# Optimization experiments

Hardware: AMD Instinct MI355X
Metric: run time of the kernel (lower is better)

## Reference

```python
import jax, jax.numpy as jnp
import numpy as np

HIDDEN = 640
NQ = 10      # query heads
NKV = 2      # kv heads
HD = HIDDEN // NQ   # 64
GROUPS = NQ // NKV  # 5
THETA = 500000.0
EPS = 1e-6


def rmsnorm(x, g):
    rms = jnp.sqrt(jnp.mean(x * x, axis=-1, keepdims=True) + EPS)
    return x / rms * g


def bitlinear(x, w, g):
    """RMSNorm + ternary weight / int8 activation fake-quant + GEMM + rescale."""
    x = rmsnorm(x, g)
    alpha = jnp.maximum(jnp.mean(jnp.abs(w)), 1e-10)
    w_q = jnp.clip(jnp.round(w / alpha), -1.0, 1.0)
    w_q = w + jax.lax.stop_gradient(w_q - w)            # STE
    gamma = jnp.maximum(jnp.max(jnp.abs(x), axis=-1, keepdims=True), 1e-10)
    x_q = jnp.clip(jnp.round(x * 127.0 / gamma), -128.0, 127.0)
    x_q = x + jax.lax.stop_gradient(x_q - x)            # STE
    return (x_q @ w_q.T) * (alpha * gamma / 127.0)


def rope_tables(L):
    # half-dim cos/sin tables [L, HD//2]; equivalent to the torch code's
    # repeat_interleave followed by [..., ::2] slicing.
    freqs = 1.0 / THETA ** (jnp.arange(0, HD, 2, dtype=jnp.float32) / HD)
    ang = jnp.arange(L, dtype=jnp.float32)[:, None] * freqs[None, :]
    return jnp.cos(ang), jnp.sin(ang)


def apply_rope(x, cos, sin):
    # x: [B,H,L,D]; cos/sin: [L,D/2] broadcast over B,H
    x1 = x[..., ::2]
    x2 = x[..., 1::2]
    o1 = x1 * cos - x2 * sin
    o2 = x2 * cos + x1 * sin
    return jnp.stack([o1, o2], axis=-1).reshape(x.shape)


def setup_inputs() -> dict:
    key = jax.random.key(0)
    ks = jax.random.split(key, 6)
    B, L = 32, 512
    x = jax.random.normal(ks[0], (B, L, HIDDEN), dtype=jnp.float32)
    s_h = 1.0 / np.sqrt(HIDDEN)
    q_w = jax.random.normal(ks[1], (NQ * HD, HIDDEN), dtype=jnp.float32) * s_h
    k_w = jax.random.normal(ks[2], (NKV * HD, HIDDEN), dtype=jnp.float32) * s_h
    v_w = jax.random.normal(ks[3], (NKV * HD, HIDDEN), dtype=jnp.float32) * s_h
    o_w = jax.random.normal(ks[4], (HIDDEN, NQ * HD), dtype=jnp.float32) * (1.0 / np.sqrt(NQ * HD))
    ones = jnp.ones((HIDDEN,), dtype=jnp.float32)
    return {
        "x": x,
        "norm_w": ones,
        "q_w": q_w, "q_g": ones,
        "k_w": k_w, "k_g": ones,
        "v_w": v_w, "v_g": ones,
        "o_w": o_w, "o_g": jnp.ones((NQ * HD,), dtype=jnp.float32),
    }


def reference(x, norm_w, q_w, q_g, k_w, k_g, v_w, v_g, o_w, o_g):
    B, L, _ = x.shape
    residual = x
    h = rmsnorm(x, norm_w)
    q = bitlinear(h, q_w, q_g).reshape(B, L, NQ, HD).transpose(0, 2, 1, 3)
    k = bitlinear(h, k_w, k_g).reshape(B, L, NKV, HD).transpose(0, 2, 1, 3)
    v = bitlinear(h, v_w, v_g).reshape(B, L, NKV, HD).transpose(0, 2, 1, 3)
    cos, sin = rope_tables(L)
    q = apply_rope(q, cos, sin)
    k = apply_rope(k, cos, sin)
    k = jnp.repeat(k, GROUPS, axis=1)   # [B,NQ,L,HD]
    v = jnp.repeat(v, GROUPS, axis=1)
    scale = 1.0 / np.sqrt(HD).astype(np.float32)
    attn = jnp.einsum("bhqd,bhkd->bhqk", q, k) * scale
    attn = jax.nn.softmax(attn, axis=-1)
    out = jnp.einsum("bhqk,bhkd->bhqd", attn, v)
    out = out.transpose(0, 2, 1, 3).reshape(B, L, NQ * HD)
    return bitlinear(out, o_w, o_g) + residual
```

## Files before the change

kernel.cpp:

```cpp
#include <hip/hip_runtime.h>
#include <math.h>
#include <stdint.h>

#define HIDDEN 640
#define NTOK   16384
#define LSEQ   512
#define BATCH  32
#define NQH    10
#define NKVH   2
#define HDIM   64
#define GROUPS 5

typedef int      int4v  __attribute__((ext_vector_type(4)));
typedef int      int16v __attribute__((ext_vector_type(16)));
typedef _Float16 f16x8  __attribute__((ext_vector_type(8)));
typedef _Float16 f16x2  __attribute__((ext_vector_type(2)));
typedef float    f32x4  __attribute__((ext_vector_type(4)));

__device__ __forceinline__ float wred_sum(float v){
  #pragma unroll
  for (int m=1;m<64;m<<=1) v += __shfl_xor(v,m);
  return v;
}
__device__ __forceinline__ float wred_max(float v){
  #pragma unroll
  for (int m=1;m<64;m<<=1) v = fmaxf(v,__shfl_xor(v,m));
  return v;
}

__device__ __forceinline__ int frag_flat(int m, int k){
  return (((m>>5)*20 + (k>>5))<<10) + (((((k>>4)&1)<<5) | (m&31))<<4) + (k&15);
}

__global__ __launch_bounds__(256) void absum4_kernel(
    const float* __restrict__ w0, const float* __restrict__ w1,
    const float* __restrict__ w2, const float* __restrict__ w3,
    float* __restrict__ sums){
  const float* w; int n;
  switch(blockIdx.y){
    case 0:  w=w0; n=640*640; break;
    case 1:  w=w1; n=128*640; break;
    case 2:  w=w2; n=128*640; break;
    default: w=w3; n=640*640; break;
  }
  __shared__ float red[256];
  int tid = threadIdx.x;
  float s = 0.f;
  for (int i = blockIdx.x*256 + tid; i < n; i += gridDim.x*256) s += fabsf(w[i]);
  red[tid] = s; __syncthreads();
  for (int off=128; off>0; off>>=1){ if (tid<off) red[tid]+=red[tid+off]; __syncthreads(); }
  if (tid==0) atomicAdd(&sums[blockIdx.y], red[0]);
}

__global__ __launch_bounds__(256) void wquant4_kernel(
    const float* __restrict__ w0, const float* __restrict__ w1,
    const float* __restrict__ w2, const float* __restrict__ w3,
    int8_t* __restrict__ o0, int8_t* __restrict__ o1,
    int8_t* __restrict__ o2, int8_t* __restrict__ o3,
    const float* __restrict__ sums){
  const float* w; int8_t* o; int n;
  switch(blockIdx.y){
    case 0:  w=w0; o=o0; n=640*640; break;
    case 1:  w=w1; o=o1; n=128*640; break;
    case 2:  w=w2; o=o2; n=128*640; break;
    default: w=w3; o=o3; n=640*640; break;
  }
  float alpha = fmaxf(sums[blockIdx.y]/(float)n, 1e-10f);
  float inva  = 1.0f/alpha;
  int i = blockIdx.x*256 + threadIdx.x;
  if (i < n){
    float t = rintf(w[i]*inva);
    t = fminf(1.f, fmaxf(-1.f, t));
    int nr = i/640;
    int kc = i - nr*640;
    o[frag_flat(nr, kc)] = (int8_t)t;
  }
}

__global__ __launch_bounds__(256) void token_prep_kernel(
    const float* __restrict__ x, const float* __restrict__ nw,
    const float* __restrict__ qg, const float* __restrict__ kg, const float* __restrict__ vg,
    int8_t* __restrict__ xqq, int8_t* __restrict__ xqk, int8_t* __restrict__ xqv,
    float* __restrict__ gq, float* __restrict__ gk, float* __restrict__ gv){
  int lane = threadIdx.x & 63;
  int m = blockIdx.x*4 + (threadIdx.x>>6);
  const float* xr = x + (size_t)m*HIDDEN;
  int abase = ((m>>5)*20480) + ((m&31)<<4)
            + ((lane>>5)<<10) + (((lane>>4)&1)<<9) + (lane&15);
  float xv[10], h[10];
  float ss = 0.f;
  #pragma unroll
  for (int j=0;j<10;j++){ float t = xr[lane + 64*j]; xv[j]=t; ss += t*t; }
  float inv1 = 1.0f/sqrtf(wred_sum(ss)*(1.0f/HIDDEN) + 1e-6f);
  float ss2 = 0.f;
  #pragma unroll
  for (int j=0;j<10;j++){ float t = xv[j]*inv1*nw[lane+64*j]; h[j]=t; ss2 += t*t; }
  float inv2 = 1.0f/sqrtf(wred_sum(ss2)*(1.0f/HIDDEN) + 1e-6f);

  const float* gs[3] = {qg, kg, vg};
  int8_t* outs[3] = {xqq, xqk, xqv};
  float* gams[3] = {gq, gk, gv};
  #pragma unroll
  for (int s=0;s<3;s++){
    const float* g = gs[s];
    float t[10], amax = 0.f;
    #pragma unroll
    for (int j=0;j<10;j++){ float v = h[j]*inv2*g[lane+64*j]; t[j]=v; amax = fmaxf(amax, fabsf(v)); }
    float gamma = fmaxf(wred_max(amax), 1e-10f);
    float sc = 127.0f/gamma;
    int8_t* dst = outs[s] + abase;
    #pragma unroll
    for (int j=0;j<10;j++){
      float v = rintf(t[j]*sc);
      v = fminf(127.f, fmaxf(-128.f, v));
      dst[j*2048] = (int8_t)v;
    }
    if (lane==0) gams[s][m] = gamma;
  }
}

__global__ __launch_bounds__(256) void o_prep_kernel(const _Float16* __restrict__ ao,
    const float* __restrict__ og, int8_t* __restrict__ xqo, float* __restrict__ go){
  int lane = threadIdx.x & 63;
  int m = blockIdx.x*4 + (threadIdx.x>>6);
  const _Float16* xr = ao + (size_t)m*HIDDEN;
  int abase = ((m>>5)*20480) + ((m&31)<<4)
            + ((lane>>5)<<10) + (((lane>>4)&1)<<9) + (lane&15);
  float xv[10];
  float ss = 0.f;
  #pragma unroll
  for (int j=0;j<10;j++){ float t = (float)xr[lane + 64*j]; xv[j]=t; ss += t*t; }
  float inv = 1.0f/sqrtf(wred_sum(ss)*(1.0f/HIDDEN) + 1e-6f);
  float t[10], amax = 0.f;
  #pragma unroll
  for (int j=0;j<10;j++){ float v = xv[j]*inv*og[lane+64*j]; t[j]=v; amax = fmaxf(amax, fabsf(v)); }
  float gamma = fmaxf(wred_max(amax), 1e-10f);
  float sc = 127.0f/gamma;
  int8_t* dst = xqo + abase;
  #pragma unroll
  for (int j=0;j<10;j++){
    float v = rintf(t[j]*sc);
    v = fminf(127.f, fmaxf(-128.f, v));
    dst[j*2048] = (int8_t)v;
  }
  if (lane==0) go[m] = gamma;
}

__device__ __forceinline__ void gemm_core(
    const int8_t* __restrict__ xq, const int8_t* __restrict__ wqf,
    int m0, int n0, int lane, int16v& acc0, int16v& acc1){
  const int8_t* a0 = xq  + (size_t)(m0>>5)*20480 + (lane<<4);
  const int8_t* b0 = wqf + (size_t)(n0>>5)*20480 + (lane<<4);
  const int8_t* b1 = b0 + 20480;
  #pragma unroll
  for (int kb=0; kb<20; kb++){
    int4v a  = *(const int4v*)(a0 + (kb<<10));
    int4v v0 = *(const int4v*)(b0 + (kb<<10));
    int4v v1 = *(const int4v*)(b1 + (kb<<10));
    acc0 = __builtin_amdgcn_mfma_i32_32x32x32_i8(a, v0, acc0, 0, 0, 0);
    acc1 = __builtin_amdgcn_mfma_i32_32x32x32_i8(a, v1, acc1, 0, 0, 0);
  }
}

__global__ __launch_bounds__(256) void qkv_gemm_kernel(
    const int8_t* __restrict__ xq_q, const float* __restrict__ g_q, const int8_t* __restrict__ wq_q,
    const int8_t* __restrict__ xq_k, const float* __restrict__ g_k, const int8_t* __restrict__ wq_k,
    const int8_t* __restrict__ xq_v, const float* __restrict__ g_v, const int8_t* __restrict__ wq_v,
    const float* __restrict__ sums,
    _Float16* __restrict__ qbuf, _Float16* __restrict__ kbuf, _Float16* __restrict__ vbuf){
  __shared__ _Float16 Tr[4][64][40];
  int bx = blockIdx.x;
  const int8_t *xq, *wq; const float* gam; _Float16* outh;
  int n0, aidx, nheads, mode; float inv_nw, vscale;
  if (bx < 10){ xq=xq_q; wq=wq_q; gam=g_q; outh=qbuf; n0=bx*64;      aidx=0; inv_nw=1.0f/409600.f; nheads=NQH;  mode=1; vscale=0.18033688011110918f; }
  else if (bx < 12){ xq=xq_k; wq=wq_k; gam=g_k; outh=kbuf; n0=(bx-10)*64; aidx=1; inv_nw=1.0f/81920.f; nheads=NKVH; mode=1; vscale=1.0f; }
  else { xq=xq_v; wq=wq_v; gam=g_v; outh=vbuf; n0=(bx-12)*64; aidx=2; inv_nw=1.0f/81920.f; nheads=NKVH; mode=2; vscale=1.0f; }

  int lane = threadIdx.x & 63;
  int w    = threadIdx.x >> 6;
  int m0   = blockIdx.y*128 + w*32;
  int half = lane >> 5, lan5 = lane & 31;

  int16v acc0 = {0}, acc1 = {0};
  gemm_core(xq, wq, m0, n0, lane, acc0, acc1);

  float alpha = fmaxf(sums[aidx]*inv_nw, 1e-10f);
  float fr0 = 0.f, fr1 = 0.f;
  if (mode == 1){
    int d0 = (lan5) & ~1;
    int d1 = (32 + lan5) & ~1;
    fr0 = __expf(-(float)d0*(1.0f/64.0f)*13.122363377404328f);
    fr1 = __expf(-(float)d1*(1.0f/64.0f)*13.122363377404328f);
  }

  #pragma unroll
  for (int reg=0; reg<16; reg++){
    int ml = (reg&3) + 8*(reg>>2) + 4*half;
    int m = m0 + ml;
    float sc = alpha*gam[m]*(1.0f/127.0f);
    float v0 = (float)acc0[reg]*sc;
    float v1 = (float)acc1[reg]*sc;
    if (mode == 1){
      int b = m >> 9, l = m & 511;
      int head = n0 >> 6;
      float p0 = __shfl_xor(v0, 1);
      float p1 = __shfl_xor(v1, 1);
      float sn0, cs0, sn1, cs1;
      __sincosf((float)l*fr0, &sn0, &cs0);
      __sincosf((float)l*fr1, &sn1, &cs1);
      if (lane & 1){ v0 = v0*cs0 + p0*sn0;  v1 = v1*cs1 + p1*sn1; }
      else         { v0 = v0*cs0 - p0*sn0;  v1 = v1*cs1 - p1*sn1; }
      _Float16* dst = outh + ((((size_t)b*nheads + head)*LSEQ + l)<<6);
      dst[lan5]      = (_Float16)(v0*vscale);
      dst[32 + lan5] = (_Float16)(v1*vscale);
    } else {
      Tr[w][lan5][ml]      = (_Float16)v0;
      Tr[w][32 + lan5][ml] = (_Float16)v1;
    }
  }
  if (mode == 2){
    int b = m0 >> 9, l0 = m0 & 511;
    int head = n0 >> 6;
    f16x8 r0 = *(const f16x8*)&Tr[w][lane][0];
    f16x8 r1 = *(const f16x8*)&Tr[w][lane][8];
    f16x8 r2 = *(const f16x8*)&Tr[w][lane][16];
    f16x8 r3 = *(const f16x8*)&Tr[w][lane][24];
    _Float16* dst = outh + (((size_t)b*nheads + head)*HDIM + lane)*LSEQ + l0;
    ((f16x8*)dst)[0] = r0;
    ((f16x8*)dst)[1] = r1;
    ((f16x8*)dst)[2] = r2;
    ((f16x8*)dst)[3] = r3;
  }
}

__global__ __launch_bounds__(256) void out_gemm_kernel(
    const int8_t* __restrict__ xq, const float* __restrict__ gam,
    const int8_t* __restrict__ wq, const float* __restrict__ sums,
    const float* __restrict__ resid, float* __restrict__ outf){
  int lane = threadIdx.x & 63;
  int w    = threadIdx.x >> 6;
  int m0   = blockIdx.y*128 + w*32;
  int n0   = blockIdx.x*64;
  int half = lane >> 5, lan5 = lane & 31;

  int16v acc0 = {0}, acc1 = {0};
  gemm_core(xq, wq, m0, n0, lane, acc0, acc1);

  float alpha = fmaxf(sums[3]*(1.0f/409600.f), 1e-10f);
  #pragma unroll
  for (int reg=0; reg<16; reg++){
    int m = m0 + (reg&3) + 8*(reg>>2) + 4*half;
    float sc = alpha*gam[m]*(1.0f/127.0f);
    size_t ofs = (size_t)m*HIDDEN;
    outf[ofs + n0 + lan5]      = (float)acc0[reg]*sc + resid[ofs + n0 + lan5];
    outf[ofs + n0 + 32 + lan5] = (float)acc1[reg]*sc + resid[ofs + n0 + 32 + lan5];
  }
}

__device__ __forceinline__ int kv_addr(int row, int chunk){
  return (row<<6) + (((chunk ^ (row&7)))<<3);
}

__device__ __forceinline__ void softmax_half(
    const f32x4* S, float& m, f32x4& lacc, f32x4* O, int quad, bool first,
    f16x8& pf0, f16x8& pf1){
  float t0 = fmaxf(fmaxf(S[0][0],S[0][1]), fmaxf(S[0][2],S[0][3]));
  float t1 = fmaxf(fmaxf(S[1][0],S[1][1]), fmaxf(S[1][2],S[1][3]));
  float t2 = fmaxf(fmaxf(S[2][0],S[2][1]), fmaxf(S[2][2],S[2][3]));
  float t3 = fmaxf(fmaxf(S[3][0],S[3][1]), fmaxf(S[3][2],S[3][3]));
  float tmax = fmaxf(fmaxf(t0,t1), fmaxf(t2,t3));
  tmax = fmaxf(tmax, __shfl_xor(tmax, 16));
  tmax = fmaxf(tmax, __shfl_xor(tmax, 32));
  float p[16];
  if (first || __any(tmax > 8.0f)){
    float delta = first ? tmax : fmaxf(tmax, 0.0f);
    m += delta;
    float af = exp2f(-delta);
    #pragma unroll
    for (int r=0;r<4;r++){
      float afr = __shfl(af, (quad<<2)+r);
      lacc[r] *= afr;
      O[0][r]*=afr; O[1][r]*=afr; O[2][r]*=afr; O[3][r]*=afr;
    }
    #pragma unroll
    for (int nt=0;nt<4;nt++){
      #pragma unroll
      for (int j=0;j<4;j++) p[(nt<<2)+j] = exp2f(S[nt][j] - delta);
    }
  } else {
    #pragma unroll
    for (int nt=0;nt<4;nt++){
      #pragma unroll
      for (int j=0;j<4;j++) p[(nt<<2)+j] = exp2f(S[nt][j]);
    }
  }
  uint32_t W[4][2];
  #pragma unroll
  for (int nt=0;nt<4;nt++){
    W[nt][0] = __builtin_bit_cast(uint32_t,
                 __builtin_amdgcn_cvt_pkrtz(p[(nt<<2)+0], p[(nt<<2)+1]));
    W[nt][1] = __builtin_bit_cast(uint32_t,
                 __builtin_amdgcn_cvt_pkrtz(p[(nt<<2)+2], p[(nt<<2)+3]));
  }
  #pragma unroll
  for (int pp=0;pp<2;pp++){
    asm volatile("v_permlane32_swap_b32 %0, %1" : "+v"(W[0][pp]), "+v"(W[1][pp]));
    asm volatile("v_permlane32_swap_b32 %0, %1" : "+v"(W[2][pp]), "+v"(W[3][pp]));
    asm volatile("v_permlane16_swap_b32 %0, %1" : "+v"(W[0][pp]), "+v"(W[1][pp]));
    asm volatile("v_permlane16_swap_b32 %0, %1" : "+v"(W[2][pp]), "+v"(W[3][pp]));
  }
  union { uint32_t u[4]; f16x8 v; } a, b;
  a.u[0]=W[0][0]; a.u[1]=W[0][1]; a.u[2]=W[1][0]; a.u[3]=W[1][1];
  b.u[0]=W[2][0]; b.u[1]=W[2][1]; b.u[2]=W[3][0]; b.u[3]=W[3][1];
  pf0 = a.v; pf1 = b.v;
}

__global__ __launch_bounds__(256,3) void attn_mfma_kernel(
    const _Float16* __restrict__ q, const _Float16* __restrict__ k,
    const _Float16* __restrict__ vt, _Float16* __restrict__ o){
  __shared__ _Float16 Ks[2][64*64];
  __shared__ _Float16 Vs[2][64*64];
  int tid  = threadIdx.x;
  int wv   = tid >> 6, lane = tid & 63;
  int quad = lane >> 4, c = lane & 15;
  int h = blockIdx.y, b = blockIdx.z;
  int hk = h / GROUPS;
  int qrow0 = blockIdx.x*128 + wv*32;

  const _Float16* qb = q + ((size_t)((b*NQH+h)*LSEQ) + qrow0 + c)*HDIM + quad*8;
  f16x8 qa0 = *(const f16x8*)qb;
  f16x8 qa1 = *(const f16x8*)(qb + 32);
  f16x8 qb0 = *(const f16x8*)(qb + 16*HDIM);
  f16x8 qb1 = *(const f16x8*)(qb + 16*HDIM + 32);

  const _Float16* kbase = k  + (size_t)((b*NKVH+hk)*LSEQ)*HDIM;
  const _Float16* vbase = vt + (size_t)((b*NKVH+hk)*HDIM)*LSEQ;

  int srow = tid >> 3, schunk = tid & 7;
  const _Float16* kg0 = kbase + (size_t)srow*HDIM      + schunk*8;
  const _Float16* kg1 = kbase + (size_t)(srow+32)*HDIM + schunk*8;
  const _Float16* vg0 = vbase + (size_t)srow*LSEQ      + schunk*8;
  const _Float16* vg1 = vbase + (size_t)(srow+32)*LSEQ + schunk*8;
  int ka0 = kv_addr(srow,    schunk);
  int ka1 = kv_addr(srow+32, schunk);

  {
    f16x8 t0 = *(const f16x8*)kg0;
    f16x8 t1 = *(const f16x8*)kg1;
    f16x8 t2 = *(const f16x8*)vg0;
    f16x8 t3 = *(const f16x8*)vg1;
    *(f16x8*)&Ks[0][ka0] = t0;
    *(f16x8*)&Ks[0][ka1] = t1;
    *(f16x8*)&Vs[0][ka0] = t2;
    *(f16x8*)&Vs[0][ka1] = t3;
  }

  f32x4 O0[4] = {{0,0,0,0},{0,0,0,0},{0,0,0,0},{0,0,0,0}};
  f32x4 O1[4] = {{0,0,0,0},{0,0,0,0},{0,0,0,0},{0,0,0,0}};
  f32x4 lacc0 = {0,0,0,0}, lacc1 = {0,0,0,0};
  float m0s = 0.f, m1s = 0.f;
  const f16x8 ones = {(_Float16)1.f,(_Float16)1.f,(_Float16)1.f,(_Float16)1.f,
                      (_Float16)1.f,(_Float16)1.f,(_Float16)1.f,(_Float16)1.f};
  f16x8 pk0, pk1, pv0, pv1;

  for (int kt=0; kt<8; kt++){
    __syncthreads();
    int cur = kt & 1, nxt = cur ^ 1;
    if (kt < 7){
      pk0 = *(const f16x8*)(kg0 + (size_t)(kt+1)*64*HDIM);
      pk1 = *(const f16x8*)(kg1 + (size_t)(kt+1)*64*HDIM);
      pv0 = *(const f16x8*)(vg0 + (kt+1)*64);
      pv1 = *(const f16x8*)(vg1 + (kt+1)*64);
    }
    f32x4 S0[4], S1[4];
    __builtin_amdgcn_s_setprio(1);
    #pragma unroll
    for (int nt=0; nt<4; nt++){
      int row = (nt<<4) + c;
      f16x8 kf0 = *(const f16x8*)&Ks[cur][kv_addr(row, quad)];
      f16x8 kf1 = *(const f16x8*)&Ks[cur][kv_addr(row, quad+4)];
      f32x4 s = {-m0s,-m0s,-m0s,-m0s};
      s = __builtin_amdgcn_mfma_f32_16x16x32_f16(kf0, qa0, s, 0,0,0);
      s = __builtin_amdgcn_mfma_f32_16x16x32_f16(kf1, qa1, s, 0,0,0);
      S0[nt] = s;
      f32x4 s2 = {-m1s,-m1s,-m1s,-m1s};
      s2 = __builtin_amdgcn_mfma_f32_16x16x32_f16(kf0, qb0, s2, 0,0,0);
      s2 = __builtin_amdgcn_mfma_f32_16x16x32_f16(kf1, qb1, s2, 0,0,0);
      S1[nt] = s2;
    }
    __builtin_amdgcn_s_setprio(0);
    f16x8 pf00, pf01, pf10, pf11;
    softmax_half(S0, m0s, lacc0, O0, quad, kt==0, pf00, pf01);
    softmax_half(S1, m1s, lacc1, O1, quad, kt==0, pf10, pf11);
    __builtin_amdgcn_s_setprio(1);
    lacc0 = __builtin_amdgcn_mfma_f32_16x16x32_f16(pf00, ones, lacc0, 0,0,0);
    lacc0 = __builtin_amdgcn_mfma_f32_16x16x32_f16(pf01, ones, lacc0, 0,0,0);
    lacc1 = __builtin_amdgcn_mfma_f32_16x16x32_f16(pf10, ones, lacc1, 0,0,0);
    lacc1 = __builtin_amdgcn_mfma_f32_16x16x32_f16(pf11, ones, lacc1, 0,0,0);
    #pragma unroll
    for (int nt=0;nt<4;nt++){
      int row = (nt<<4) + c;
      f16x8 vf0 = *(const f16x8*)&Vs[cur][kv_addr(row, quad)];
      f16x8 vf1 = *(const f16x8*)&Vs[cur][kv_addr(row, quad+4)];
      O0[nt] = __builtin_amdgcn_mfma_f32_16x16x32_f16(pf00, vf0, O0[nt], 0,0,0);
      O0[nt] = __builtin_amdgcn_mfma_f32_16x16x32_f16(pf01, vf1, O0[nt], 0,0,0);
      O1[nt] = __builtin_amdgcn_mfma_f32_16x16x32_f16(pf10, vf0, O1[nt], 0,0,0);
      O1[nt] = __builtin_amdgcn_mfma_f32_16x16x32_f16(pf11, vf1, O1[nt], 0,0,0);
    }
    __builtin_amdgcn_s_setprio(0);
    if (kt < 7){
      *(f16x8*)&Ks[nxt][ka0] = pk0;
      *(f16x8*)&Ks[nxt][ka1] = pk1;
      *(f16x8*)&Vs[nxt][ka0] = pv0;
      *(f16x8*)&Vs[nxt][ka1] = pv1;
    }
  }
  #pragma unroll
  for (int r=0;r<4;r++){
    float invl0 = 1.0f/lacc0[r];
    float invl1 = 1.0f/lacc1[r];
    int m0 = (b<<9) + qrow0 + (quad<<2) + r;
    _Float16* d0 = o + (size_t)m0*HIDDEN + (h<<6);
    _Float16* d1 = o + (size_t)(m0+16)*HIDDEN + (h<<6);
    #pragma unroll
    for (int nt=0;nt<4;nt++){
      d0[(nt<<4)+c] = (_Float16)(O0[nt][r]*invl0);
      d1[(nt<<4)+c] = (_Float16)(O1[nt][r]*invl1);
    }
  }
}

extern "C" void kernel_launch(void* const* d_in, const int* in_sizes, int n_in,
                              void* d_out, int out_size, void* d_ws, size_t ws_size,
                              hipStream_t stream){
  (void)in_sizes; (void)n_in; (void)out_size; (void)ws_size;
  const float* x  = (const float*)d_in[0];
  const float* nw = (const float*)d_in[1];
  const float* qw = (const float*)d_in[2];
  const float* qg = (const float*)d_in[3];
  const float* kw = (const float*)d_in[4];
  const float* kg = (const float*)d_in[5];
  const float* vw = (const float*)d_in[6];
  const float* vg = (const float*)d_in[7];
  const float* ow = (const float*)d_in[8];
  const float* og = (const float*)d_in[9];
  float* out = (float*)d_out;

  char* base = (char*)d_ws;
  size_t off = 0;
  auto alloc = [&](size_t nbytes)->void*{
    off = (off + 255) & ~(size_t)255;
    void* p = base + off;
    off += nbytes;
    return p;
  };
  float*  sums = (float*) alloc(4*sizeof(float));
  int8_t* wq_q = (int8_t*)alloc(640*640);
  int8_t* wq_k = (int8_t*)alloc(128*640);
  int8_t* wq_v = (int8_t*)alloc(128*640);
  int8_t* wq_o = (int8_t*)alloc(640*640);
  int8_t* xq_q = (int8_t*)alloc((size_t)NTOK*HIDDEN);
  int8_t* xq_k = (int8_t*)alloc((size_t)NTOK*HIDDEN);
  int8_t* xq_v = (int8_t*)alloc((size_t)NTOK*HIDDEN);
  int8_t* xq_o = (int8_t*)alloc((size_t)NTOK*HIDDEN);
  float*  g_q  = (float*) alloc((size_t)NTOK*4);
  float*  g_k  = (float*) alloc((size_t)NTOK*4);
  float*  g_v  = (float*) alloc((size_t)NTOK*4);
  float*  g_o  = (float*) alloc((size_t)NTOK*4);
  _Float16* qbuf = (_Float16*)alloc((size_t)BATCH*NQH *LSEQ*HDIM*2);
  _Float16* kbuf = (_Float16*)alloc((size_t)BATCH*NKVH*LSEQ*HDIM*2);
  _Float16* vbuf = (_Float16*)alloc((size_t)BATCH*NKVH*LSEQ*HDIM*2);
  _Float16* abuf = (_Float16*)alloc((size_t)NTOK*HIDDEN*2);

  (void)hipMemsetAsync(sums, 0, 4*sizeof(float), stream);
  absum4_kernel<<<dim3(64,4),256,0,stream>>>(qw, kw, vw, ow, sums);
  wquant4_kernel<<<dim3(1600,4),256,0,stream>>>(qw, kw, vw, ow, wq_q, wq_k, wq_v, wq_o, sums);

  token_prep_kernel<<<NTOK/4,256,0,stream>>>(x, nw, qg, kg, vg, xq_q, xq_k, xq_v, g_q, g_k, g_v);

  qkv_gemm_kernel<<<dim3(14,128),256,0,stream>>>(xq_q, g_q, wq_q,
                                                 xq_k, g_k, wq_k,
                                                 xq_v, g_v, wq_v,
                                                 sums, qbuf, kbuf, vbuf);

  attn_mfma_kernel<<<dim3(4,NQH,BATCH),256,0,stream>>>(qbuf, kbuf, vbuf, abuf);

  o_prep_kernel<<<NTOK/4,256,0,stream>>>(abuf, og, xq_o, g_o);
  out_gemm_kernel<<<dim3(10,128),256,0,stream>>>(xq_o, g_o, wq_o, sums, x, out);
}
```

Before: 238.2 us.

## Software-pipeline attention QK and softmax-PV, stage K/V via direct global-to-LDS loads

Restructures the attention loop so the QK^T MFMAs for tile kt overlap the softmax and PV MFMAs of tile kt-1, using a triple-buffered V tile and a deferred max-shift correction term. K/V staging now uses global_load_lds to write straight into shared memory, with a swizzled source address, instead of going through registers. The intent is to hide softmax VALU latency behind MFMA work and to cut register pressure and VGPR round trips on loads. In exchange it uses more LDS and adds extra softmax branching, which may lower occupancy.

After: 266.4 us. 11.8% more time.

```diff
diff --git a/kernel.cpp b/kernel.cpp
--- a/kernel.cpp
+++ b/kernel.cpp
@@ -261,20 +261,30 @@
   return (row<<6) + (((chunk ^ (row&7)))<<3);
 }
 
+__device__ __forceinline__ void gload_lds16(const void* g, void* l){
+  __builtin_amdgcn_global_load_lds(
+      (const __attribute__((address_space(1))) unsigned int*)g,
+      (__attribute__((address_space(3))) unsigned int*)l, 16, 0, 0);
+}
+
 __device__ __forceinline__ void softmax_half(
-    const f32x4* S, float& m, f32x4& lacc, f32x4* O, int quad, bool first,
+    const f32x4* S, float& m, float& dc, f32x4& lacc, f32x4* O, int quad, bool first,
     f16x8& pf0, f16x8& pf1){
-  float t0 = fmaxf(fmaxf(S[0][0],S[0][1]), fmaxf(S[0][2],S[0][3]));
-  float t1 = fmaxf(fmaxf(S[1][0],S[1][1]), fmaxf(S[1][2],S[1][3]));
-  float t2 = fmaxf(fmaxf(S[2][0],S[2][1]), fmaxf(S[2][2],S[2][3]));
-  float t3 = fmaxf(fmaxf(S[3][0],S[3][1]), fmaxf(S[3][2],S[3][3]));
-  float tmax = fmaxf(fmaxf(t0,t1), fmaxf(t2,t3));
+  float t0 = fmaxf(fmaxf(fmaxf(S[0][0],S[0][1]),S[0][2]),S[0][3]);
+  float t1 = fmaxf(fmaxf(fmaxf(S[1][0],S[1][1]),S[1][2]),S[1][3]);
+  float t2 = fmaxf(fmaxf(fmaxf(S[2][0],S[2][1]),S[2][2]),S[2][3]);
+  float t3 = fmaxf(fmaxf(fmaxf(S[3][0],S[3][1]),S[3][2]),S[3][3]);
+  float tmax = fmaxf(fmaxf(fmaxf(t0,t1),t2),t3);
   tmax = fmaxf(tmax, __shfl_xor(tmax, 16));
   tmax = fmaxf(tmax, __shfl_xor(tmax, 32));
+  float D = dc;
+  float teff = tmax - D;
   float p[16];
-  if (first || __any(tmax > 8.0f)){
-    float delta = first ? tmax : fmaxf(tmax, 0.0f);
+  if (first || __any(teff > 8.0f)){
+    float delta = first ? teff : fmaxf(teff, 0.0f);
+    float shift = D + delta;
     m += delta;
+    dc = delta;
     float af = exp2f(-delta);
     #pragma unroll
     for (int r=0;r<4;r++){
@@ -285,9 +295,17 @@
     #pragma unroll
     for (int nt=0;nt<4;nt++){
       #pragma unroll
-      for (int j=0;j<4;j++) p[(nt<<2)+j] = exp2f(S[nt][j] - delta);
+      for (int j=0;j<4;j++) p[(nt<<2)+j] = exp2f(S[nt][j] - shift);
+    }
+  } else if (__any(D != 0.0f)){
+    dc = 0.0f;
+    #pragma unroll
+    for (int nt=0;nt<4;nt++){
+      #pragma unroll
+      for (int j=0;j<4;j++) p[(nt<<2)+j] = exp2f(S[nt][j] - D);
     }
   } else {
+    dc = 0.0f;
     #pragma unroll
     for (int nt=0;nt<4;nt++){
       #pragma unroll
@@ -319,7 +337,7 @@
     const _Float16* __restrict__ q, const _Float16* __restrict__ k,
     const _Float16* __restrict__ vt, _Float16* __restrict__ o){
   __shared__ _Float16 Ks[2][64*64];
-  __shared__ _Float16 Vs[2][64*64];
+  __shared__ _Float16 Vs[3][64*64];
   int tid  = threadIdx.x;
   int wv   = tid >> 6, lane = tid & 63;
   int quad = lane >> 4, c = lane & 15;
@@ -333,46 +351,39 @@
   f16x8 qb0 = *(const f16x8*)(qb + 16*HDIM);
   f16x8 qb1 = *(const f16x8*)(qb + 16*HDIM + 32);
 
-  const _Float16* kbase = k  + (size_t)((b*NKVH+hk)*LSEQ)*HDIM;
-  const _Float16* vbase = vt + (size_t)((b*NKVH+hk)*HDIM)*LSEQ;
-
-  int srow = tid >> 3, schunk = tid & 7;
-  const _Float16* kg0 = kbase + (size_t)srow*HDIM      + schunk*8;
-  const _Float16* kg1 = kbase + (size_t)(srow+32)*HDIM + schunk*8;
-  const _Float16* vg0 = vbase + (size_t)srow*LSEQ      + schunk*8;
-  const _Float16* vg1 = vbase + (size_t)(srow+32)*LSEQ + schunk*8;
-  int ka0 = kv_addr(srow,    schunk);
-  int ka1 = kv_addr(srow+32, schunk);
-
-  {
-    f16x8 t0 = *(const f16x8*)kg0;
-    f16x8 t1 = *(const f16x8*)kg1;
-    f16x8 t2 = *(const f16x8*)vg0;
-    f16x8 t3 = *(const f16x8*)vg1;
-    *(f16x8*)&Ks[0][ka0] = t0;
-    *(f16x8*)&Ks[0][ka1] = t1;
-    *(f16x8*)&Vs[0][ka0] = t2;
-    *(f16x8*)&Vs[0][ka1] = t3;
-  }
+  const char* kbase = (const char*)(k  + (size_t)((b*NKVH+hk)*LSEQ)*HDIM);
+  const char* vbase = (const char*)(vt + (size_t)((b*NKVH+hk)*HDIM)*LSEQ);
+
+  int r7 = lane >> 3, s7 = lane & 7;
+  int cg = s7 ^ r7;
+  size_t koffA = (size_t)(wv*8 + r7)*128  + (size_t)cg*16;
+  size_t koffB = koffA + 32*128;
+  size_t voffA = (size_t)(wv*8 + r7)*1024 + (size_t)cg*16;
+  size_t voffB = voffA + 32*1024;
+
+  #define STAGE_KV(ksl, vsl, t) do{                                          \
+    gload_lds16(kbase + (size_t)(t)*8192 + koffA, &Ks[ksl][wv*512]);         \
+    gload_lds16(kbase + (size_t)(t)*8192 + koffB, &Ks[ksl][2048 + wv*512]);  \
+    gload_lds16(vbase + (size_t)(t)*128  + voffA, &Vs[vsl][wv*512]);         \
+    gload_lds16(vbase + (size_t)(t)*128  + voffB, &Vs[vsl][2048 + wv*512]);  \
+  }while(0)
+
+  STAGE_KV(0, 0, 0);
 
   f32x4 O0[4] = {{0,0,0,0},{0,0,0,0},{0,0,0,0},{0,0,0,0}};
   f32x4 O1[4] = {{0,0,0,0},{0,0,0,0},{0,0,0,0},{0,0,0,0}};
   f32x4 lacc0 = {0,0,0,0}, lacc1 = {0,0,0,0};
-  float m0s = 0.f, m1s = 0.f;
+  float m0s = 0.f, m1s = 0.f, dc0 = 0.f, dc1 = 0.f;
   const f16x8 ones = {(_Float16)1.f,(_Float16)1.f,(_Float16)1.f,(_Float16)1.f,
                       (_Float16)1.f,(_Float16)1.f,(_Float16)1.f,(_Float16)1.f};
-  f16x8 pk0, pk1, pv0, pv1;
-
+  f32x4 Sp0[4], Sp1[4];
+
+  #pragma unroll
   for (int kt=0; kt<8; kt++){
     __syncthreads();
-    int cur = kt & 1, nxt = cur ^ 1;
-    if (kt < 7){
-      pk0 = *(const f16x8*)(kg0 + (size_t)(kt+1)*64*HDIM);
-      pk1 = *(const f16x8*)(kg1 + (size_t)(kt+1)*64*HDIM);
-      pv0 = *(const f16x8*)(vg0 + (kt+1)*64);
-      pv1 = *(const f16x8*)(vg1 + (kt+1)*64);
-    }
-    f32x4 S0[4], S1[4];
+    if (kt < 7) STAGE_KV((kt+1)&1, (kt+1)%3, kt+1);
+    int cur = kt & 1;
+    f32x4 Sn0[4], Sn1[4];
     __builtin_amdgcn_s_setprio(1);
     #pragma unroll
     for (int nt=0; nt<4; nt++){
@@ -382,17 +393,42 @@
       f32x4 s = {-m0s,-m0s,-m0s,-m0s};
       s = __builtin_amdgcn_mfma_f32_16x16x32_f16(kf0, qa0, s, 0,0,0);
       s = __builtin_amdgcn_mfma_f32_16x16x32_f16(kf1, qa1, s, 0,0,0);
-      S0[nt] = s;
+      Sn0[nt] = s;
       f32x4 s2 = {-m1s,-m1s,-m1s,-m1s};
       s2 = __builtin_amdgcn_mfma_f32_16x16x32_f16(kf0, qb0, s2, 0,0,0);
       s2 = __builtin_amdgcn_mfma_f32_16x16x32_f16(kf1, qb1, s2, 0,0,0);
-      S1[nt] = s2;
+      Sn1[nt] = s2;
     }
     __builtin_amdgcn_s_setprio(0);
+    if (kt > 0){
+      int prv = (kt-1)%3;
+      f16x8 pf00, pf01, pf10, pf11;
+      softmax_half(Sp0, m0s, dc0, lacc0, O0, quad, kt==1, pf00, pf01);
+      softmax_half(Sp1, m1s, dc1, lacc1, O1, quad, kt==1, pf10, pf11);
+      __builtin_amdgcn_s_setprio(1);
+      lacc0 = __builtin_amdgcn_mfma_f32_16x16x32_f16(pf00, ones, lacc0, 0,0,0);
+      lacc0 = __builtin_amdgcn_mfma_f32_16x16x32_f16(pf01, ones, lacc0, 0,0,0);
+      lacc1 = __builtin_amdgcn_mfma_f32_16x16x32_f16(pf10, ones, lacc1, 0,0,0);
+      lacc1 = __builtin_amdgcn_mfma_f32_16x16x32_f16(pf11, ones, lacc1, 0,0,0);
+      #pragma unroll
+      for (int nt=0;nt<4;nt++){
+        int row = (nt<<4) + c;
+        f16x8 vf0 = *(const f16x8*)&Vs[prv][kv_addr(row, quad)];
+        f16x8 vf1 = *(const f16x8*)&Vs[prv][kv_addr(row, quad+4)];
+        O0[nt] = __builtin_amdgcn_mfma_f32_16x16x32_f16(pf00, vf0, O0[nt], 0,0,0);
+        O0[nt] = __builtin_amdgcn_mfma_f32_16x16x32_f16(pf01, vf1, O0[nt], 0,0,0);
+        O1[nt] = __builtin_amdgcn_mfma_f32_16x16x32_f16(pf10, vf0, O1[nt], 0,0,0);
+        O1[nt] = __builtin_amdgcn_mfma_f32_16x16x32_f16(pf11, vf1, O1[nt], 0,0,0);
+      }
+      __builtin_amdgcn_s_setprio(0);
+    }
+    #pragma unroll
+    for (int nt=0;nt<4;nt++){ Sp0[nt] = Sn0[nt]; Sp1[nt] = Sn1[nt]; }
+  }
+  {
     f16x8 pf00, pf01, pf10, pf11;
-    softmax_half(S0, m0s, lacc0, O0, quad, kt==0, pf00, pf01);
-    softmax_half(S1, m1s, lacc1, O1, quad, kt==0, pf10, pf11);
-    __builtin_amdgcn_s_setprio(1);
+    softmax_half(Sp0, m0s, dc0, lacc0, O0, quad, false, pf00, pf01);
+    softmax_half(Sp1, m1s, dc1, lacc1, O1, quad, false, pf10, pf11);
     lacc0 = __builtin_amdgcn_mfma_f32_16x16x32_f16(pf00, ones, lacc0, 0,0,0);
     lacc0 = __builtin_amdgcn_mfma_f32_16x16x32_f16(pf01, ones, lacc0, 0,0,0);
     lacc1 = __builtin_amdgcn_mfma_f32_16x16x32_f16(pf10, ones, lacc1, 0,0,0);
@@ -400,21 +436,15 @@
     #pragma unroll
     for (int nt=0;nt<4;nt++){
       int row = (nt<<4) + c;
-      f16x8 vf0 = *(const f16x8*)&Vs[cur][kv_addr(row, quad)];
-      f16x8 vf1 = *(const f16x8*)&Vs[cur][kv_addr(row, quad+4)];
+      f16x8 vf0 = *(const f16x8*)&Vs[1][kv_addr(row, quad)];
+      f16x8 vf1 = *(const f16x8*)&Vs[1][kv_addr(row, quad+4)];
       O0[nt] = __builtin_amdgcn_mfma_f32_16x16x32_f16(pf00, vf0, O0[nt], 0,0,0);
       O0[nt] = __builtin_amdgcn_mfma_f32_16x16x32_f16(pf01, vf1, O0[nt], 0,0,0);
       O1[nt] = __builtin_amdgcn_mfma_f32_16x16x32_f16(pf10, vf0, O1[nt], 0,0,0);
       O1[nt] = __builtin_amdgcn_mfma_f32_16x16x32_f16(pf11, vf1, O1[nt], 0,0,0);
     }
-    __builtin_amdgcn_s_setprio(0);
-    if (kt < 7){
-      *(f16x8*)&Ks[nxt][ka0] = pk0;
-      *(f16x8*)&Ks[nxt][ka1] = pk1;
-      *(f16x8*)&Vs[nxt][ka0] = pv0;
-      *(f16x8*)&Vs[nxt][ka1] = pv1;
-    }
-  }
+  }
+  #undef STAGE_KV
   #pragma unroll
   for (int r=0;r<4;r++){
     float invl0 = 1.0f/lacc0[r];
```

## Stage K/V tiles with direct global-to-LDS loads and defer softmax max reduction

Applied to the files above, without the earlier changes.

The attention kernel's double-buffered K/V staging now uses global_load_lds DMA loads straight into shared memory instead of loading into registers and writing to LDS later. The XOR swizzle is kept by permuting the global source chunk per lane. This frees VGPRs and removes the ds_write instructions from the loop. The cross-lane row-max shuffles in the softmax move inside the rarely taken rescale branch, and the trigger check now uses per-lane partial maxima. The risk is relying on the compiler to insert correct vmcnt waits before the barrier for the LDS-DMA loads.

Measured after the change: 242.7 us. Within noise of the previous version (+1.9%).

```diff
diff --git a/kernel.cpp b/kernel.cpp
--- a/kernel.cpp
+++ b/kernel.cpp
@@ -261,6 +261,12 @@
   return (row<<6) + (((chunk ^ (row&7)))<<3);
 }
 
+__device__ __forceinline__ void gload_lds16(const void* g, void* l){
+  __builtin_amdgcn_global_load_lds(
+      (const __attribute__((address_space(1))) unsigned int*)g,
+      (__attribute__((address_space(3))) unsigned int*)l, 16, 0, 0);
+}
+
 __device__ __forceinline__ void softmax_half(
     const f32x4* S, float& m, f32x4& lacc, f32x4* O, int quad, bool first,
     f16x8& pf0, f16x8& pf1){
@@ -269,11 +275,11 @@
   float t2 = fmaxf(fmaxf(S[2][0],S[2][1]), fmaxf(S[2][2],S[2][3]));
   float t3 = fmaxf(fmaxf(S[3][0],S[3][1]), fmaxf(S[3][2],S[3][3]));
   float tmax = fmaxf(fmaxf(t0,t1), fmaxf(t2,t3));
-  tmax = fmaxf(tmax, __shfl_xor(tmax, 16));
-  tmax = fmaxf(tmax, __shfl_xor(tmax, 32));
   float p[16];
   if (first || __any(tmax > 8.0f)){
-    float delta = first ? tmax : fmaxf(tmax, 0.0f);
+    float rmax = fmaxf(tmax, __shfl_xor(tmax, 16));
+    rmax = fmaxf(rmax, __shfl_xor(rmax, 32));
+    float delta = first ? rmax : fmaxf(rmax, 0.0f);
     m += delta;
     float af = exp2f(-delta);
     #pragma unroll
@@ -333,27 +339,24 @@
   f16x8 qb0 = *(const f16x8*)(qb + 16*HDIM);
   f16x8 qb1 = *(const f16x8*)(qb + 16*HDIM + 32);
 
-  const _Float16* kbase = k  + (size_t)((b*NKVH+hk)*LSEQ)*HDIM;
-  const _Float16* vbase = vt + (size_t)((b*NKVH+hk)*HDIM)*LSEQ;
-
-  int srow = tid >> 3, schunk = tid & 7;
-  const _Float16* kg0 = kbase + (size_t)srow*HDIM      + schunk*8;
-  const _Float16* kg1 = kbase + (size_t)(srow+32)*HDIM + schunk*8;
-  const _Float16* vg0 = vbase + (size_t)srow*LSEQ      + schunk*8;
-  const _Float16* vg1 = vbase + (size_t)(srow+32)*LSEQ + schunk*8;
-  int ka0 = kv_addr(srow,    schunk);
-  int ka1 = kv_addr(srow+32, schunk);
-
-  {
-    f16x8 t0 = *(const f16x8*)kg0;
-    f16x8 t1 = *(const f16x8*)kg1;
-    f16x8 t2 = *(const f16x8*)vg0;
-    f16x8 t3 = *(const f16x8*)vg1;
-    *(f16x8*)&Ks[0][ka0] = t0;
-    *(f16x8*)&Ks[0][ka1] = t1;
-    *(f16x8*)&Vs[0][ka0] = t2;
-    *(f16x8*)&Vs[0][ka1] = t3;
-  }
+  const char* kbase = (const char*)(k  + (size_t)((b*NKVH+hk)*LSEQ)*HDIM);
+  const char* vbase = (const char*)(vt + (size_t)((b*NKVH+hk)*HDIM)*LSEQ);
+
+  int r7 = lane >> 3, s7 = lane & 7;
+  int cg = s7 ^ r7;
+  size_t koffA = (size_t)(wv*8 + r7)*128  + (size_t)cg*16;
+  size_t koffB = koffA + 32*128;
+  size_t voffA = (size_t)(wv*8 + r7)*1024 + (size_t)cg*16;
+  size_t voffB = voffA + 32*1024;
+
+  #define STAGE_KV(sl, t) do{                                              \
+    gload_lds16(kbase + (size_t)(t)*8192 + koffA, &Ks[sl][wv*512]);        \
+    gload_lds16(kbase + (size_t)(t)*8192 + koffB, &Ks[sl][2048 + wv*512]); \
+    gload_lds16(vbase + (size_t)(t)*128  + voffA, &Vs[sl][wv*512]);        \
+    gload_lds16(vbase + (size_t)(t)*128  + voffB, &Vs[sl][2048 + wv*512]); \
+  }while(0)
+
+  STAGE_KV(0, 0);
 
   f32x4 O0[4] = {{0,0,0,0},{0,0,0,0},{0,0,0,0},{0,0,0,0}};
   f32x4 O1[4] = {{0,0,0,0},{0,0,0,0},{0,0,0,0},{0,0,0,0}};
@@ -361,17 +364,11 @@
   float m0s = 0.f, m1s = 0.f;
   const f16x8 ones = {(_Float16)1.f,(_Float16)1.f,(_Float16)1.f,(_Float16)1.f,
                       (_Float16)1.f,(_Float16)1.f,(_Float16)1.f,(_Float16)1.f};
-  f16x8 pk0, pk1, pv0, pv1;
 
   for (int kt=0; kt<8; kt++){
     __syncthreads();
-    int cur = kt & 1, nxt = cur ^ 1;
-    if (kt < 7){
-      pk0 = *(const f16x8*)(kg0 + (size_t)(kt+1)*64*HDIM);
-      pk1 = *(const f16x8*)(kg1 + (size_t)(kt+1)*64*HDIM);
-      pv0 = *(const f16x8*)(vg0 + (kt+1)*64);
-      pv1 = *(const f16x8*)(vg1 + (kt+1)*64);
-    }
+    int cur = kt & 1;
+    if (kt < 7) STAGE_KV(cur^1, kt+1);
     f32x4 S0[4], S1[4];
     __builtin_amdgcn_s_setprio(1);
     #pragma unroll
@@ -408,13 +405,8 @@
       O1[nt] = __builtin_amdgcn_mfma_f32_16x16x32_f16(pf11, vf1, O1[nt], 0,0,0);
     }
     __builtin_amdgcn_s_setprio(0);
-    if (kt < 7){
-      *(f16x8*)&Ks[nxt][ka0] = pk0;
-      *(f16x8*)&Ks[nxt][ka1] = pk1;
-      *(f16x8*)&Vs[nxt][ka0] = pv0;
-      *(f16x8*)&Vs[nxt][ka1] = pv1;
-    }
-  }
+  }
+  #undef STAGE_KV
   #pragma unroll
   for (int r=0;r<4;r++){
     float invl0 = 1.0f/lacc0[r];
```
